# Kernel optimization log

Measured on AMD Instinct MI355X. Metric: run time of the kernel, lower is better.

The kernel has to match this reference:

```python
import jax, jax.numpy as jnp
import numpy as np

P, M, N, E = 128, 128, 50000, 800000
KAPPA = 0.99  # kappa / A_rho with A_rho = 1.0


def setup_inputs() -> dict:
    key = jax.random.key(0)
    ks = jax.random.split(key, 7)
    stdv = 1.0 / np.sqrt(M)
    U = jax.random.normal(ks[0], (P, N), jnp.float32)
    edge_rows = jax.random.randint(ks[1], (E,), 0, N, dtype=jnp.int32)
    edge_cols = jax.random.randint(ks[2], (E,), 0, N, dtype=jnp.int32)
    # roughly row-normalized adjacency values (avg degree 16)
    edge_vals = jax.random.uniform(ks[3], (E,), jnp.float32) / 16.0
    W = jax.random.uniform(ks[4], (M, M), jnp.float32, -stdv, stdv)
    Omega_1 = jax.random.uniform(ks[5], (M, P), jnp.float32, -stdv, stdv)
    Omega_2 = jax.random.uniform(ks[6], (M, P), jnp.float32, -stdv, stdv)
    return dict(U=U, edge_rows=edge_rows, edge_cols=edge_cols, edge_vals=edge_vals,
                W=W, Omega_1=Omega_1, Omega_2=Omega_2, fw_mitr=20)


def _proj_norm_inf(W, kappa):
    # Project each row of W onto the l1-ball of radius kappa (=> ||W||_inf <= kappa),
    # only for rows whose l1 norm exceeds kappa (matches IGNN projection_norm_inf).
    absW = jnp.abs(W)
    row_sum = absW.sum(-1)
    u = jnp.sort(absW, axis=-1)[:, ::-1]              # descending per row
    css = jnp.cumsum(u, axis=-1) - kappa
    k = jnp.arange(1, W.shape[-1] + 1, dtype=W.dtype)
    rho = jnp.sum((u - css / k) > 0, axis=-1) - 1      # last valid index
    theta = jnp.take_along_axis(css, rho[:, None], axis=-1)[:, 0]
    theta = jnp.maximum(theta / (rho + 1).astype(W.dtype), 0.0)
    proj = jnp.sign(W) * jnp.maximum(absW - theta[:, None], 0.0)
    return jnp.where((row_sum > kappa)[:, None], proj, W)


def _spmm_At(edge_rows, edge_cols, edge_vals, Mnm, n):
    # (A^T @ Mnm)[i] = sum over edges (r,c,v): v * Mnm[r] scattered to row c
    return jax.ops.segment_sum(edge_vals[:, None] * Mnm[edge_rows], edge_cols,
                               num_segments=n)


def reference(U, edge_rows, edge_cols, edge_vals, W, Omega_1, Omega_2, fw_mitr):
    n = U.shape[1]
    Wp = _proj_norm_inf(W, KAPPA)
    # b_Omega = (A^T @ (Omega_1 @ U)^T)^T + Omega_2 @ U   -> shape (m, n)
    s1 = Omega_1 @ U                                       # (m, n)
    s1 = _spmm_At(edge_rows, edge_cols, edge_vals, s1.T, n).T
    B = s1 + Omega_2 @ U

    def step(X, _):
        Xw = Wp @ X                                        # dense (m,m)@(m,n)
        sup = _spmm_At(edge_rows, edge_cols, edge_vals, Xw.T, n).T
        return jax.nn.relu(sup + B), None                  # phi = ReLU

    X_out, _ = jax.lax.scan(step, B, None, length=fw_mitr)  # X_0 = B
    return X_out
```

## Files before the change

kernel.cpp:

```cpp
#include <hip/hip_runtime.h>

#define NN 50000
#define EE 800000
#define ITERS 20
#define KAPPA 0.99f
#define NTILES 3125
#define NB1 196

typedef __bf16 bf16x8 __attribute__((ext_vector_type(8)));
typedef float f32x4 __attribute__((ext_vector_type(4)));
typedef unsigned short u16;
typedef unsigned int u32;

__device__ __forceinline__ u16 f2bf(float f) {
  u32 u = __float_as_uint(f);
  u32 r = u + 0x7FFFu + ((u >> 16) & 1u);
  return (u16)(r >> 16);
}
__device__ __forceinline__ u32 pack2bf(float a, float b) {
  return (u32)f2bf(a) | ((u32)f2bf(b) << 16);
}
__device__ __forceinline__ float bflo(u32 x) { return __uint_as_float(x << 16); }
__device__ __forceinline__ float bfhi(u32 x) { return __uint_as_float(x & 0xFFFF0000u); }

__global__ __launch_bounds__(128)
void proj_w(const float* __restrict__ W, u16* __restrict__ Wb) {
  __shared__ float su[128];
  __shared__ float scs[128];
  __shared__ int sred[128];
  __shared__ float theta_s, rowsum_s;
  int row = blockIdx.x, t = threadIdx.x;
  float w = W[row * 128 + t];
  float aw = fabsf(w);
  su[t] = aw;
  __syncthreads();
  for (int k = 2; k <= 128; k <<= 1) {
    for (int j = k >> 1; j > 0; j >>= 1) {
      int ixj = t ^ j;
      if (ixj > t) {
        float a = su[t], b = su[ixj];
        if ((t & k) == 0) { if (a > b) { su[t] = b; su[ixj] = a; } }
        else              { if (a < b) { su[t] = b; su[ixj] = a; } }
      }
      __syncthreads();
    }
  }
  float ud = su[127 - t];
  scs[t] = ud;
  __syncthreads();
  for (int off = 1; off < 128; off <<= 1) {
    float v = (t >= off) ? scs[t - off] : 0.f;
    __syncthreads();
    scs[t] += v;
    __syncthreads();
  }
  float cs = scs[t] - KAPPA;
  sred[t] = ((ud - cs / (float)(t + 1)) > 0.f) ? 1 : 0;
  __syncthreads();
  for (int off = 64; off > 0; off >>= 1) {
    if (t < off) sred[t] += sred[t + off];
    __syncthreads();
  }
  if (t == 0) {
    int rho = sred[0] - 1;
    float th = (scs[rho] - KAPPA) / (float)(rho + 1);
    theta_s = fmaxf(th, 0.f);
    rowsum_s = scs[127];
  }
  __syncthreads();
  float outv;
  if (rowsum_s > KAPPA) {
    float pw = fmaxf(aw - theta_s, 0.f);
    outv = (w >= 0.f) ? pw : -pw;
  } else {
    outv = w;
  }
  Wb[row * 128 + t] = f2bf(outv);
}

__global__ __launch_bounds__(256)
void convert_mat(const float* __restrict__ a, u16* __restrict__ o, int count) {
  int i = blockIdx.x * 256 + threadIdx.x;
  if (i < count) o[i] = f2bf(a[i]);
}

__global__ __launch_bounds__(256)
void transpose_u(const float* __restrict__ U, u16* __restrict__ Ub, int Nn) {
  __shared__ u16 sh[64][130];
  int n0 = blockIdx.x * 64;
  int t = threadIdx.x;
  int nl = t & 63, pq = t >> 6;
  #pragma unroll
  for (int i = 0; i < 128; i += 4) {
    int p = i + pq;
    int n = n0 + nl;
    float v = (n < Nn) ? U[(size_t)p * Nn + n] : 0.f;
    sh[nl][p] = f2bf(v);
  }
  __syncthreads();
  #pragma unroll
  for (int j = 0; j < 16; ++j) {
    int node = j * 4 + pq;
    int n = n0 + node;
    if (n < Nn) {
      u32 lo = sh[node][nl * 2], hi = sh[node][nl * 2 + 1];
      ((u32*)Ub)[(size_t)n * 64 + nl] = lo | (hi << 16);
    }
  }
}

__global__ __launch_bounds__(256)
void hist_k(const int* __restrict__ cols, int* __restrict__ counts) {
  int i = blockIdx.x * 256 + threadIdx.x;
  atomicAdd(&counts[cols[i]], 1);
}

__global__ __launch_bounds__(256)
void scan1(const int* __restrict__ counts, int* __restrict__ bsums) {
  __shared__ int s[256];
  int t = threadIdx.x;
  int i = blockIdx.x * 256 + t;
  s[t] = (i < NN) ? counts[i] : 0;
  __syncthreads();
  for (int off = 128; off > 0; off >>= 1) {
    if (t < off) s[t] += s[t + off];
    __syncthreads();
  }
  if (t == 0) bsums[blockIdx.x] = s[0];
}

__global__ __launch_bounds__(256)
void scan2(const int* __restrict__ bsums, int* __restrict__ boffs) {
  __shared__ int s[256];
  int t = threadIdx.x;
  int v = (t < NB1) ? bsums[t] : 0;
  s[t] = v;
  __syncthreads();
  for (int off = 1; off < 256; off <<= 1) {
    int u = (t >= off) ? s[t - off] : 0;
    __syncthreads();
    s[t] += u;
    __syncthreads();
  }
  if (t < NB1) boffs[t] = s[t] - v;
}

__global__ __launch_bounds__(256)
void scan3(const int* __restrict__ counts, const int* __restrict__ boffs,
           int* __restrict__ colptr, int* __restrict__ cursor) {
  __shared__ int s[256];
  int t = threadIdx.x;
  int i = blockIdx.x * 256 + t;
  int v = (i < NN) ? counts[i] : 0;
  s[t] = v;
  __syncthreads();
  for (int off = 1; off < 256; off <<= 1) {
    int u = (t >= off) ? s[t - off] : 0;
    __syncthreads();
    s[t] += u;
    __syncthreads();
  }
  int excl = s[t] - v + boffs[blockIdx.x];
  if (i < NN) { colptr[i] = excl; cursor[i] = excl; }
  if (i == 0) colptr[NN] = EE;
}

__global__ __launch_bounds__(256)
void scatter_k(const int* __restrict__ rows, const int* __restrict__ cols,
               const float* __restrict__ vals, int* __restrict__ cursor,
               uint2* __restrict__ rv) {
  int i = blockIdx.x * 256 + threadIdx.x;
  int c = cols[i];
  int pos = atomicAdd(&cursor[c], 1);
  rv[pos] = make_uint2((u32)rows[i], __float_as_uint(vals[i]));
}

__global__ __launch_bounds__(256, 2)
void gemm_k(const u16* __restrict__ Mb, const u16* __restrict__ Xsrc,
            u32* __restrict__ outp) {
  int lane = threadIdx.x & 63;
  int wid = threadIdx.x >> 6;
  int r = lane & 15, kg = lane >> 4;
  bf16x8 wf[8][4];
  #pragma unroll
  for (int mt = 0; mt < 8; ++mt)
    #pragma unroll
    for (int kk = 0; kk < 4; ++kk)
      wf[mt][kk] = *reinterpret_cast<const bf16x8*>(
          Mb + (mt * 16 + r) * 128 + kk * 32 + kg * 8);
  const int nw = gridDim.x * 4;
  int t = blockIdx.x * 4 + wid;
  if (t >= NTILES) return;
  bf16x8 xc[4], xn[4];
  {
    const u16* xp = Xsrc + (size_t)(t * 16 + r) * 128 + kg * 8;
    #pragma unroll
    for (int kk = 0; kk < 4; ++kk)
      xc[kk] = *reinterpret_cast<const bf16x8*>(xp + kk * 32);
  }
  while (true) {
    int nxt = t + nw;
    bool has = (nxt < NTILES);
    if (has) {
      const u16* xp = Xsrc + (size_t)(nxt * 16 + r) * 128 + kg * 8;
      #pragma unroll
      for (int kk = 0; kk < 4; ++kk)
        xn[kk] = *reinterpret_cast<const bf16x8*>(xp + kk * 32);
    }
    f32x4 acc[8];
    #pragma unroll
    for (int mt = 0; mt < 8; ++mt) acc[mt] = (f32x4)(0.f);
    #pragma unroll
    for (int mt = 0; mt < 8; ++mt)
      #pragma unroll
      for (int kk = 0; kk < 4; ++kk)
        acc[mt] = __builtin_amdgcn_mfma_f32_16x16x32_bf16(
            wf[mt][kk], xc[kk], acc[mt], 0, 0, 0);
    u32* o = outp + (size_t)(t * 16 + r) * 64 + kg * 2;
    #pragma unroll
    for (int mt = 0; mt < 8; ++mt) {
      uint2 pk;
      pk.x = pack2bf(acc[mt][0], acc[mt][1]);
      pk.y = pack2bf(acc[mt][2], acc[mt][3]);
      *reinterpret_cast<uint2*>(o + mt * 8) = pk;
    }
    if (!has) break;
    #pragma unroll
    for (int kk = 0; kk < 4; ++kk) xc[kk] = xn[kk];
    t = nxt;
  }
}

template<int MODE>
__global__ __launch_bounds__(256, 8)
void spmm_k(const int* __restrict__ colptr, const uint2* __restrict__ rv,
            const u16* __restrict__ Src, u32* __restrict__ Bb,
            u32* __restrict__ Xb, float* __restrict__ Xf) {
  int n = (blockIdx.x << 2) + (threadIdx.x >> 6);
  int lane = threadIdx.x & 63;
  int beg = colptr[n];
  int end = colptr[n + 1];
  int deg = end - beg;
  const u16* sp = Src + (lane << 1);
  float a0 = 0.f, a1 = 0.f, c0 = 0.f, c1 = 0.f;
  if (deg > 0) {
    if (deg <= 64) {
      uint2 p = rv[beg + ((lane < deg) ? lane : 0)];
      int rr = (int)p.x;
      float vv = __uint_as_float(p.y);
      int e = 0;
      for (; e + 8 <= deg; e += 8) {
        int ri[8]; u32 xi[8]; float vi[8];
        #pragma unroll
        for (int j = 0; j < 8; ++j) ri[j] = __shfl(rr, e + j);
        #pragma unroll
        for (int j = 0; j < 8; ++j) xi[j] = *(const u32*)(sp + ri[j] * 128);
        #pragma unroll
        for (int j = 0; j < 8; ++j) vi[j] = __shfl(vv, e + j);
        #pragma unroll
        for (int j = 0; j < 8; ++j) {
          if (j & 1) { c0 += vi[j] * bflo(xi[j]); c1 += vi[j] * bfhi(xi[j]); }
          else       { a0 += vi[j] * bflo(xi[j]); a1 += vi[j] * bfhi(xi[j]); }
        }
      }
      for (; e < deg; ++e) {
        int re = __shfl(rr, e);
        float ve = __shfl(vv, e);
        u32 x = *(const u32*)(sp + re * 128);
        a0 += ve * bflo(x); a1 += ve * bfhi(x);
      }
    } else {
      for (int e = beg; e < end; ++e) {
        uint2 p = rv[e];
        u32 x = *(const u32*)(sp + (int)p.x * 128);
        float v = __uint_as_float(p.y);
        a0 += v * bflo(x); a1 += v * bfhi(x);
      }
    }
  }
  a0 += c0; a1 += c1;
  u32 bp = Bb[(size_t)n * 64 + lane];
  float o0 = a0 + bflo(bp), o1 = a1 + bfhi(bp);
  if (MODE >= 1) { o0 = fmaxf(o0, 0.f); o1 = fmaxf(o1, 0.f); }
  if (MODE == 0) Bb[(size_t)n * 64 + lane] = pack2bf(o0, o1);
  if (MODE == 1) Xb[(size_t)n * 64 + lane] = pack2bf(o0, o1);
  if (MODE == 2)
    *(float2*)(Xf + (size_t)n * 128 + (lane << 1)) = make_float2(o0, o1);
}

__global__ __launch_bounds__(256)
void transpose_out(const float* __restrict__ Xf, float* __restrict__ out, int Nn) {
  __shared__ float sh[128][65];
  int n0 = blockIdx.x * 64;
  int t = threadIdx.x;
  #pragma unroll
  for (int i = 0; i < 32; ++i) {
    int idx = i * 256 + t;
    int node = idx >> 7, m = idx & 127;
    int n = n0 + node;
    float v = (n < Nn) ? Xf[(size_t)n * 128 + m] : 0.f;
    sh[m][node] = v;
  }
  __syncthreads();
  #pragma unroll
  for (int i = 0; i < 32; ++i) {
    int idx = i * 256 + t;
    int m = idx >> 6, nl = idx & 63;
    int n = n0 + nl;
    if (n < Nn) out[(size_t)m * Nn + n] = sh[m][nl];
  }
}

extern "C" void kernel_launch(void* const* d_in, const int* in_sizes, int n_in,
                              void* d_out, int out_size, void* d_ws, size_t ws_size,
                              hipStream_t stream) {
  (void)in_sizes; (void)n_in; (void)out_size; (void)ws_size;
  const float* U   = (const float*)d_in[0];
  const int*   er  = (const int*)d_in[1];
  const int*   ec  = (const int*)d_in[2];
  const float* ev  = (const float*)d_in[3];
  const float* W   = (const float*)d_in[4];
  const float* Om1 = (const float*)d_in[5];
  const float* Om2 = (const float*)d_in[6];
  float* out = (float*)d_out;

  char* base = (char*)d_ws;
  size_t off = 0;
  auto alloc = [&](size_t b) {
    char* p = base + off;
    off = (off + b + 255) & ~(size_t)255;
    return p;
  };
  u16* Wb     = (u16*)alloc(128 * 128 * 2);
  u16* Om1b   = (u16*)alloc(128 * 128 * 2);
  u16* Om2b   = (u16*)alloc(128 * 128 * 2);
  float* Xf   = (float*)alloc((size_t)NN * 128 * 4);
  u16* Ub     = (u16*)Xf;
  u32* Xb     = (u32*)alloc((size_t)NN * 64 * 4);
  u32* Xwb    = (u32*)alloc((size_t)NN * 64 * 4);
  u32* Bb     = (u32*)alloc((size_t)NN * 64 * 4);
  int* counts = (int*)alloc((size_t)NN * 4);
  int* colptr = (int*)alloc((size_t)(NN + 1) * 4);
  int* cursor = (int*)alloc((size_t)NN * 4);
  int* bsums  = (int*)alloc((size_t)NB1 * 4);
  int* boffs  = (int*)alloc((size_t)NB1 * 4);
  uint2* rv   = (uint2*)alloc((size_t)EE * 8);

  proj_w<<<dim3(128), dim3(128), 0, stream>>>(W, Wb);
  convert_mat<<<dim3(64), dim3(256), 0, stream>>>(Om1, Om1b, 128 * 128);
  convert_mat<<<dim3(64), dim3(256), 0, stream>>>(Om2, Om2b, 128 * 128);
  transpose_u<<<dim3((NN + 63) / 64), dim3(256), 0, stream>>>(U, Ub, NN);
  hipMemsetAsync(counts, 0, (size_t)NN * 4, stream);
  hist_k<<<dim3(EE / 256), dim3(256), 0, stream>>>(ec, counts);
  scan1<<<dim3(NB1), dim3(256), 0, stream>>>(counts, bsums);
  scan2<<<dim3(1), dim3(256), 0, stream>>>(bsums, boffs);
  scan3<<<dim3(NB1), dim3(256), 0, stream>>>(counts, boffs, colptr, cursor);
  scatter_k<<<dim3(EE / 256), dim3(256), 0, stream>>>(er, ec, ev, cursor, rv);

  gemm_k<<<dim3(512), dim3(256), 0, stream>>>(Om1b, Ub, Xwb);
  gemm_k<<<dim3(512), dim3(256), 0, stream>>>(Om2b, Ub, Bb);
  spmm_k<0><<<dim3(NN / 4), dim3(256), 0, stream>>>(colptr, rv, (const u16*)Xwb,
                                                    Bb, (u32*)nullptr, (float*)nullptr);

  for (int it = 0; it < ITERS; ++it) {
    const u16* xsrc = (it == 0) ? (const u16*)Bb : (const u16*)Xb;
    gemm_k<<<dim3(512), dim3(256), 0, stream>>>(Wb, xsrc, Xwb);
    if (it < ITERS - 1)
      spmm_k<1><<<dim3(NN / 4), dim3(256), 0, stream>>>(colptr, rv, (const u16*)Xwb,
                                                        Bb, Xb, (float*)nullptr);
    else
      spmm_k<2><<<dim3(NN / 4), dim3(256), 0, stream>>>(colptr, rv, (const u16*)Xwb,
                                                        Bb, (u32*)nullptr, Xf);
  }

  transpose_out<<<dim3((NN + 63) / 64), dim3(256), 0, stream>>>(Xf, out, NN);
}
```

Before: 1.285 ms.

## Process four nodes per wavefront in SpMM with 16-byte gathers, multipass scatter

The SpMM kernel now assigns 16 lanes per destination node, so four nodes share a wavefront. Each lane gathers 8 bf16 values with one 16-byte load instead of a 4-byte load, which cuts wasted lanes on low-degree nodes and raises memory-level parallelism. The CSR scatter now runs in 8 passes over destination-column ranges to localise the atomic cursor updates and writes, at the cost of reading the edge arrays 8 times. The two Omega conversion kernels are also merged into one launch.

```diff
diff --git a/kernel.cpp b/kernel.cpp
--- a/kernel.cpp
+++ b/kernel.cpp
@@ -6,6 +6,9 @@
 #define KAPPA 0.99f
 #define NTILES 3125
 #define NB1 196
+#define SC_PASSES 8
+#define SC_BLOCKS (EE / 256)
+#define SC_RANGE (NN / SC_PASSES)
 
 typedef __bf16 bf16x8 __attribute__((ext_vector_type(8)));
 typedef float f32x4 __attribute__((ext_vector_type(4)));
@@ -79,9 +82,11 @@
 }
 
 __global__ __launch_bounds__(256)
-void convert_mat(const float* __restrict__ a, u16* __restrict__ o, int count) {
+void convert_mat2(const float* __restrict__ a, const float* __restrict__ b,
+                  u16* __restrict__ oa, u16* __restrict__ ob) {
   int i = blockIdx.x * 256 + threadIdx.x;
-  if (i < count) o[i] = f2bf(a[i]);
+  if (i < 16384) oa[i] = f2bf(a[i]);
+  else           ob[i - 16384] = f2bf(b[i - 16384]);
 }
 
 __global__ __launch_bounds__(256)
@@ -169,10 +174,14 @@
 void scatter_k(const int* __restrict__ rows, const int* __restrict__ cols,
                const float* __restrict__ vals, int* __restrict__ cursor,
                uint2* __restrict__ rv) {
-  int i = blockIdx.x * 256 + threadIdx.x;
+  int pass = blockIdx.x / SC_BLOCKS;
+  int i = (blockIdx.x % SC_BLOCKS) * 256 + threadIdx.x;
   int c = cols[i];
-  int pos = atomicAdd(&cursor[c], 1);
-  rv[pos] = make_uint2((u32)rows[i], __float_as_uint(vals[i]));
+  int lo = pass * SC_RANGE;
+  if (c >= lo && c < lo + SC_RANGE) {
+    int pos = atomicAdd(&cursor[c], 1);
+    rv[pos] = make_uint2((u32)rows[i], __float_as_uint(vals[i]));
+  }
 }
 
 __global__ __launch_bounds__(256, 2)
@@ -236,56 +245,71 @@
 void spmm_k(const int* __restrict__ colptr, const uint2* __restrict__ rv,
             const u16* __restrict__ Src, u32* __restrict__ Bb,
             u32* __restrict__ Xb, float* __restrict__ Xf) {
-  int n = (blockIdx.x << 2) + (threadIdx.x >> 6);
+  int wid = threadIdx.x >> 6;
   int lane = threadIdx.x & 63;
+  int l16 = lane & 15;
+  int gb = lane & 48;
+  int n = blockIdx.x * 16 + wid * 4 + (lane >> 4);
   int beg = colptr[n];
-  int end = colptr[n + 1];
-  int deg = end - beg;
-  const u16* sp = Src + (lane << 1);
-  float a0 = 0.f, a1 = 0.f, c0 = 0.f, c1 = 0.f;
-  if (deg > 0) {
-    if (deg <= 64) {
-      uint2 p = rv[beg + ((lane < deg) ? lane : 0)];
-      int rr = (int)p.x;
-      float vv = __uint_as_float(p.y);
-      int e = 0;
-      for (; e + 8 <= deg; e += 8) {
-        int ri[8]; u32 xi[8]; float vi[8];
-        #pragma unroll
-        for (int j = 0; j < 8; ++j) ri[j] = __shfl(rr, e + j);
-        #pragma unroll
-        for (int j = 0; j < 8; ++j) xi[j] = *(const u32*)(sp + ri[j] * 128);
-        #pragma unroll
-        for (int j = 0; j < 8; ++j) vi[j] = __shfl(vv, e + j);
-        #pragma unroll
-        for (int j = 0; j < 8; ++j) {
-          if (j & 1) { c0 += vi[j] * bflo(xi[j]); c1 += vi[j] * bfhi(xi[j]); }
-          else       { a0 += vi[j] * bflo(xi[j]); a1 += vi[j] * bfhi(xi[j]); }
-        }
+  int deg = colptr[n + 1] - beg;
+  const u32* sp = (const u32*)Src + l16 * 4;
+  float a0 = 0.f, a1 = 0.f, a2 = 0.f, a3 = 0.f;
+  float a4 = 0.f, a5 = 0.f, a6 = 0.f, a7 = 0.f;
+  for (int base = 0; base < deg; base += 16) {
+    int cnt = deg - base; if (cnt > 16) cnt = 16;
+    uint2 p = rv[beg + base + ((l16 < cnt) ? l16 : 0)];
+    int rr = (int)p.x;
+    float vv = __uint_as_float(p.y);
+    int j = 0;
+    for (; j + 4 <= cnt; j += 4) {
+      int ri[4]; float vi[4]; uint4 xr[4];
+      #pragma unroll
+      for (int q = 0; q < 4; ++q) ri[q] = __shfl(rr, gb + j + q);
+      #pragma unroll
+      for (int q = 0; q < 4; ++q)
+        xr[q] = *(const uint4*)(sp + (size_t)ri[q] * 64);
+      #pragma unroll
+      for (int q = 0; q < 4; ++q) vi[q] = __shfl(vv, gb + j + q);
+      #pragma unroll
+      for (int q = 0; q < 4; ++q) {
+        a0 += vi[q] * bflo(xr[q].x); a1 += vi[q] * bfhi(xr[q].x);
+        a2 += vi[q] * bflo(xr[q].y); a3 += vi[q] * bfhi(xr[q].y);
+        a4 += vi[q] * bflo(xr[q].z); a5 += vi[q] * bfhi(xr[q].z);
+        a6 += vi[q] * bflo(xr[q].w); a7 += vi[q] * bfhi(xr[q].w);
       }
-      for (; e < deg; ++e) {
-        int re = __shfl(rr, e);
-        float ve = __shfl(vv, e);
-        u32 x = *(const u32*)(sp + re * 128);
-        a0 += ve * bflo(x); a1 += ve * bfhi(x);
-      }
-    } else {
-      for (int e = beg; e < end; ++e) {
-        uint2 p = rv[e];
-        u32 x = *(const u32*)(sp + (int)p.x * 128);
-        float v = __uint_as_float(p.y);
-        a0 += v * bflo(x); a1 += v * bfhi(x);
-      }
-    }
-  }
-  a0 += c0; a1 += c1;
-  u32 bp = Bb[(size_t)n * 64 + lane];
-  float o0 = a0 + bflo(bp), o1 = a1 + bfhi(bp);
-  if (MODE >= 1) { o0 = fmaxf(o0, 0.f); o1 = fmaxf(o1, 0.f); }
-  if (MODE == 0) Bb[(size_t)n * 64 + lane] = pack2bf(o0, o1);
-  if (MODE == 1) Xb[(size_t)n * 64 + lane] = pack2bf(o0, o1);
-  if (MODE == 2)
-    *(float2*)(Xf + (size_t)n * 128 + (lane << 1)) = make_float2(o0, o1);
+    }
+    for (; j < cnt; ++j) {
+      int re = __shfl(rr, gb + j);
+      float ve = __shfl(vv, gb + j);
+      uint4 x = *(const uint4*)(sp + (size_t)re * 64);
+      a0 += ve * bflo(x.x); a1 += ve * bfhi(x.x);
+      a2 += ve * bflo(x.y); a3 += ve * bfhi(x.y);
+      a4 += ve * bflo(x.z); a5 += ve * bfhi(x.z);
+      a6 += ve * bflo(x.w); a7 += ve * bfhi(x.w);
+    }
+  }
+  uint4 bp = *(const uint4*)(Bb + (size_t)n * 64 + l16 * 4);
+  float o0 = a0 + bflo(bp.x), o1 = a1 + bfhi(bp.x);
+  float o2 = a2 + bflo(bp.y), o3 = a3 + bfhi(bp.y);
+  float o4 = a4 + bflo(bp.z), o5 = a5 + bfhi(bp.z);
+  float o6 = a6 + bflo(bp.w), o7 = a7 + bfhi(bp.w);
+  if (MODE >= 1) {
+    o0 = fmaxf(o0, 0.f); o1 = fmaxf(o1, 0.f);
+    o2 = fmaxf(o2, 0.f); o3 = fmaxf(o3, 0.f);
+    o4 = fmaxf(o4, 0.f); o5 = fmaxf(o5, 0.f);
+    o6 = fmaxf(o6, 0.f); o7 = fmaxf(o7, 0.f);
+  }
+  if (MODE <= 1) {
+    uint4 pk;
+    pk.x = pack2bf(o0, o1); pk.y = pack2bf(o2, o3);
+    pk.z = pack2bf(o4, o5); pk.w = pack2bf(o6, o7);
+    u32* dst = (MODE == 0) ? Bb : Xb;
+    *(uint4*)(dst + (size_t)n * 64 + l16 * 4) = pk;
+  } else {
+    float* xo = Xf + (size_t)n * 128 + l16 * 8;
+    *(float4*)(xo)     = make_float4(o0, o1, o2, o3);
+    *(float4*)(xo + 4) = make_float4(o4, o5, o6, o7);
+  }
 }
 
 __global__ __launch_bounds__(256)
@@ -347,30 +371,29 @@
   uint2* rv   = (uint2*)alloc((size_t)EE * 8);
 
   proj_w<<<dim3(128), dim3(128), 0, stream>>>(W, Wb);
-  convert_mat<<<dim3(64), dim3(256), 0, stream>>>(Om1, Om1b, 128 * 128);
-  convert_mat<<<dim3(64), dim3(256), 0, stream>>>(Om2, Om2b, 128 * 128);
+  convert_mat2<<<dim3(128), dim3(256), 0, stream>>>(Om1, Om2, Om1b, Om2b);
   transpose_u<<<dim3((NN + 63) / 64), dim3(256), 0, stream>>>(U, Ub, NN);
   hipMemsetAsync(counts, 0, (size_t)NN * 4, stream);
   hist_k<<<dim3(EE / 256), dim3(256), 0, stream>>>(ec, counts);
   scan1<<<dim3(NB1), dim3(256), 0, stream>>>(counts, bsums);
   scan2<<<dim3(1), dim3(256), 0, stream>>>(bsums, boffs);
   scan3<<<dim3(NB1), dim3(256), 0, stream>>>(counts, boffs, colptr, cursor);
-  scatter_k<<<dim3(EE / 256), dim3(256), 0, stream>>>(er, ec, ev, cursor, rv);
+  scatter_k<<<dim3(SC_PASSES * SC_BLOCKS), dim3(256), 0, stream>>>(er, ec, ev, cursor, rv);
 
   gemm_k<<<dim3(512), dim3(256), 0, stream>>>(Om1b, Ub, Xwb);
   gemm_k<<<dim3(512), dim3(256), 0, stream>>>(Om2b, Ub, Bb);
-  spmm_k<0><<<dim3(NN / 4), dim3(256), 0, stream>>>(colptr, rv, (const u16*)Xwb,
-                                                    Bb, (u32*)nullptr, (float*)nullptr);
+  spmm_k<0><<<dim3(NN / 16), dim3(256), 0, stream>>>(colptr, rv, (const u16*)Xwb,
+                                                     Bb, (u32*)nullptr, (float*)nullptr);
 
   for (int it = 0; it < ITERS; ++it) {
     const u16* xsrc = (it == 0) ? (const u16*)Bb : (const u16*)Xb;
     gemm_k<<<dim3(512), dim3(256), 0, stream>>>(Wb, xsrc, Xwb);
     if (it < ITERS - 1)
-      spmm_k<1><<<dim3(NN / 4), dim3(256), 0, stream>>>(colptr, rv, (const u16*)Xwb,
-                                                        Bb, Xb, (float*)nullptr);
+      spmm_k<1><<<dim3(NN / 16), dim3(256), 0, stream>>>(colptr, rv, (const u16*)Xwb,
+                                                         Bb, Xb, (float*)nullptr);
     else
-      spmm_k<2><<<dim3(NN / 4), dim3(256), 0, stream>>>(colptr, rv, (const u16*)Xwb,
-                                                        Bb, (u32*)nullptr, Xf);
+      spmm_k<2><<<dim3(NN / 16), dim3(256), 0, stream>>>(colptr, rv, (const u16*)Xwb,
+                                                         Bb, (u32*)nullptr, Xf);
   }
 
   transpose_out<<<dim3((NN + 63) / 64), dim3(256), 0, stream>>>(Xf, out, NN);
```

Measured after the change: 1.221 ms. 5.0% less time.
